# Performance work log

Hardware: AMD Instinct MI355X
Metric: run time of the kernel (lower is better)

The kernel has to match this reference:

```python
import jax, jax.numpy as jnp
import numpy as np

T, H, W = 64, 1024, 1024
GRAD_PCT = 0.15
BZ_PCT = 0.3      # 30th percentile of |Bz|


def setup_inputs() -> dict:
    key = jax.random.key(0)
    k1, k2, k3 = jax.random.split(key, 3)
    frames = jax.random.normal(k1, (T, H, W), dtype=jnp.float32)
    observed_mask = jnp.ones((T,), dtype=bool)
    conv_w = jax.random.normal(k2, (4, 1, 3), dtype=jnp.float32) * 0.3  # depthwise OIH
    conv_b = jax.random.normal(k3, (4,), dtype=jnp.float32) * 0.1
    return {"frames": frames, "observed_mask": observed_mask,
            "conv_w": conv_w, "conv_b": conv_b}


def _pil_stats(frames):
    # frames: [T,H,W] -> stats [T,4] (length, intensity, x_centroid, y_centroid)
    T_, H_, W_ = frames.shape
    N = H_ * W_
    gx = jnp.pad(frames[:, :, 1:] - frames[:, :, :-1], ((0, 0), (0, 0), (0, 1)))
    gy = jnp.pad(frames[:, 1:, :] - frames[:, :-1, :], ((0, 0), (0, 1), (0, 0)))
    gm = jnp.sqrt(gx * gx + gy * gy)                    # [T,H,W]
    gm_flat = gm.reshape(T_, N)
    thr = jnp.sort(gm_flat, axis=-1)[:, int((1.0 - GRAD_PCT) * (N - 1))]
    bz_abs = jnp.abs(frames).reshape(T_, N)
    bz_thr = jnp.sort(bz_abs, axis=-1)[:, int(BZ_PCT * (N - 1))]
    mask = ((gm_flat > thr[:, None]) & (bz_abs < bz_thr[:, None])).astype(frames.dtype)
    pil_sum = jnp.clip(mask.sum(-1), 1e-6)
    length = pil_sum / N
    intensity = (gm_flat * mask).sum(-1) / pil_sum
    w3 = (mask * gm_flat).reshape(T_, H_, W_)           # centroid weights
    wsum = jnp.clip(w3.sum((1, 2)), 1e-6)
    xs = jnp.arange(W_, dtype=frames.dtype)
    ys = jnp.arange(H_, dtype=frames.dtype)
    x_cent = jnp.einsum('thw,w->t', w3, xs) / wsum / W_
    y_cent = jnp.einsum('thw,h->t', w3, ys) / wsum / H_
    return jnp.stack([length, intensity, x_cent, y_cent], axis=-1)


def reference(frames, observed_mask, conv_w, conv_b):
    # observed_mask is all-True -> all T frames observed (static n_obs = T)
    n = frames.shape[0]
    stats = _pil_stats(frames)                          # [T,4]
    x = stats.T[None]                                   # [1,4,T]
    y = jax.lax.conv_general_dilated(
        x, conv_w, window_strides=(1,), padding=((1, 1),),
        feature_group_count=4, dimension_numbers=('NCH', 'OIH', 'NCH'))
    s = (y + conv_b[None, :, None])[0].T                # [T,4] smoothed
    length, intensity, x_cent, y_cent = s[:, 0], s[:, 1], s[:, 2], s[:, 3]
    length_mean = length.mean()
    intensity_mean = intensity.mean()
    t_norm = jnp.linspace(0.0, 1.0, n)
    length_trend = ((length - length_mean) * (t_norm - 0.5)).sum() * 6 / n
    intensity_trend = ((intensity - intensity_mean) * (t_norm - 0.5)).sum() * 6 / n
    dx = x_cent[1:] - x_cent[:-1]
    dy = y_cent[1:] - y_cent[:-1]
    speeds = jnp.sqrt(dx * dx + dy * dy)
    motion_speed = speeds.mean()
    motion_direction = jnp.arctan2(dy.sum(), dx.sum()) / np.pi
    growth_rate = (length[-1] - length[0]) / max(1, n - 1)
    instability = jnp.std(speeds, ddof=1)               # unbiased, per-step speeds
    return jnp.stack([length_mean, length_trend, intensity_mean, intensity_trend,
                      motion_speed, motion_direction, growth_rate, instability])
```

## Files before the change

kernel.cpp:

```cpp
#include <hip/hip_runtime.h>
#include <math.h>
#include <stddef.h>

constexpr int T_ = 64;
constexpr int H_ = 1024;
constexpr int W_ = 1024;
constexpr int N_ = H_ * W_;
constexpr unsigned RANK_G = 891288;
constexpr unsigned RANK_B = 314572;

constexpr int ROWS_PER_BLOCK = 32;
constexpr int BLOCKS_PER_FRAME = H_ / ROWS_PER_BLOCK;

constexpr int SROWS = 16;
constexpr int NS = SROWS * W_;
constexpr int SHB = 8192;
constexpr int MARGIN = 192;
constexpr int RS_G = (int)(RANK_G / 64);
constexpr int RS_B = (int)(RANK_B / 64);

constexpr unsigned CAPG = 1536;
constexpr unsigned CAPB = 1536;
constexpr unsigned CAPX = 448;

constexpr unsigned CACHE_N = 26624;
constexpr int SEL_THREADS = 512;

constexpr int RES_SPLIT = 8;

struct WS {
  unsigned lo[2][T_], hi[2][T_];
  unsigned cntG[T_][32], cntB[T_][32], cntX[T_][32];
  unsigned cbG[T_][32], cbB[T_][32];
  float    thr[2][T_];
  double   part[T_][32][4];
  double   acc2[T_][RES_SPLIT][4];
  unsigned Gg[T_][32][CAPG];
  unsigned Ga[T_][32][CAPG];
  unsigned Bb[T_][32][CAPB];
  unsigned Xg[T_][32][CAPX];
  unsigned Xb[T_][32][CAPX];
  unsigned Xa[T_][32][CAPX];
};

__device__ __forceinline__ float gm_at(float cur, float right, float down,
                                       int col, int row) {
  float gx = (col < W_ - 1) ? (right - cur) : 0.0f;
  float gy = (row < H_ - 1) ? (down - cur) : 0.0f;
  return sqrtf(gx * gx + gy * gy);
}

__global__ __launch_bounds__(256) void sample_kernel(const float* __restrict__ frames,
                                                     WS* ws) {
  const int t = blockIdx.x;
  __shared__ unsigned hist[2][SHB];
  __shared__ unsigned sub[4][1024];
  __shared__ unsigned partial[256], chunk_before[256];
  __shared__ unsigned selB[4], selCB[4];
  const int tx = threadIdx.x, c = tx * 4;
  for (int i = tx; i < 2 * SHB; i += 256) (&hist[0][0])[i] = 0;
  for (int i = tx; i < 4 * 1024; i += 256) (&sub[0][0])[i] = 0;
  __syncthreads();
  const float* f = frames + (size_t)t * N_;

  for (int r = 0; r < SROWS; ++r) {
    const int h = r * 64 + 32;
    const float* row = f + (size_t)h * W_;
    float4 a = *(const float4*)(row + c);
    float an = (c + 4 < W_) ? row[c + 4] : 0.0f;
    float4 b = *(const float4*)(row + W_ + c);
    float xs[5] = {a.x, a.y, a.z, a.w, an};
    float ys[4] = {b.x, b.y, b.z, b.w};
#pragma unroll
    for (int j = 0; j < 4; ++j) {
      float gm = gm_at(xs[j], xs[j + 1], ys[j], c + j, h);
      float bz = fabsf(xs[j]);
      atomicAdd(&hist[0][__float_as_uint(gm) >> 18], 1u);
      atomicAdd(&hist[1][__float_as_uint(bz) >> 18], 1u);
    }
  }
  __syncthreads();

  for (int q = 0; q < 2; ++q) {
    unsigned s = 0;
    for (int j = 0; j < SHB / 256; ++j) s += hist[q][tx * (SHB / 256) + j];
    partial[tx] = s;
    __syncthreads();
    if (tx == 0) {
      unsigned cum = 0;
      for (int i = 0; i < 256; ++i) { chunk_before[i] = cum; cum += partial[i]; }
    }
    __syncthreads();
    for (int e = 0; e < 2; ++e) {
      int k = (q == 0 ? RS_G : RS_B) + (e == 0 ? -MARGIN : MARGIN);
      unsigned cb = chunk_before[tx];
      if ((unsigned)k >= cb && (unsigned)k < cb + partial[tx]) {
        unsigned rem = (unsigned)k - cb, cum = 0;
        for (int j = 0; j < SHB / 256; ++j) {
          unsigned hv = hist[q][tx * (SHB / 256) + j];
          if (rem < cum + hv) {
            selB[q * 2 + e]  = tx * (SHB / 256) + j;
            selCB[q * 2 + e] = cb + cum;
            break;
          }
          cum += hv;
        }
      }
    }
    __syncthreads();
  }

  for (int r = 0; r < SROWS; ++r) {
    const int h = r * 64 + 32;
    const float* row = f + (size_t)h * W_;
    float4 a = *(const float4*)(row + c);
    float an = (c + 4 < W_) ? row[c + 4] : 0.0f;
    float4 b = *(const float4*)(row + W_ + c);
    float xs[5] = {a.x, a.y, a.z, a.w, an};
    float ys[4] = {b.x, b.y, b.z, b.w};
#pragma unroll
    for (int j = 0; j < 4; ++j) {
      float gm = gm_at(xs[j], xs[j + 1], ys[j], c + j, h);
      float bz = fabsf(xs[j]);
      unsigned ug = __float_as_uint(gm), ub = __float_as_uint(bz);
#pragma unroll
      for (int e = 0; e < 2; ++e) {
        if ((ug >> 18) == selB[e])     atomicAdd(&sub[e][(ug >> 8) & 1023u], 1u);
        if ((ub >> 18) == selB[2 + e]) atomicAdd(&sub[2 + e][(ub >> 8) & 1023u], 1u);
      }
    }
  }
  __syncthreads();

  for (int qe = 0; qe < 4; ++qe) {
    unsigned s = 0;
    for (int j = 0; j < 4; ++j) s += sub[qe][tx * 4 + j];
    partial[tx] = s;
    __syncthreads();
    if (tx == 0) {
      unsigned cum = 0;
      for (int i = 0; i < 256; ++i) { chunk_before[i] = cum; cum += partial[i]; }
    }
    __syncthreads();
    int q = qe >> 1, e = qe & 1;
    int k0 = (q == 0 ? RS_G : RS_B) + (e == 0 ? -MARGIN : MARGIN);
    unsigned k = (unsigned)k0 - selCB[qe];
    unsigned cb = chunk_before[tx];
    if (k >= cb && k < cb + partial[tx]) {
      unsigned rem = k - cb, cum = 0;
      for (int j = 0; j < 4; ++j) {
        unsigned hv = sub[qe][tx * 4 + j];
        if (rem < cum + hv) {
          unsigned sb = tx * 4 + j;
          unsigned bound = (selB[qe] << 18) | (sb << 8);
          if (e == 0) ws->lo[q][t] = bound;
          else        ws->hi[q][t] = bound + 256u;
          break;
        }
        cum += hv;
      }
    }
    __syncthreads();
  }
}

__global__ __launch_bounds__(256) void main_kernel(const float* __restrict__ frames,
                                                   WS* ws) {
  const int t = blockIdx.y, blk = blockIdx.x, r0 = blk * ROWS_PER_BLOCK;
  const unsigned lg = ws->lo[0][t], hg = ws->hi[0][t];
  const unsigned lb = ws->lo[1][t], hb = ws->hi[1][t];
  __shared__ unsigned cnt[3];
  const int tx = threadIdx.x, c = tx * 4, lane = tx & 63, wave = tx >> 6;
  if (tx < 3) cnt[tx] = 0;
  __syncthreads();
  unsigned* __restrict__ Gg = ws->Gg[t][blk];
  unsigned* __restrict__ Ga = ws->Ga[t][blk];
  unsigned* __restrict__ Bb = ws->Bb[t][blk];
  unsigned* __restrict__ Xg = ws->Xg[t][blk];
  unsigned* __restrict__ Xb = ws->Xb[t][blk];
  unsigned* __restrict__ Xa = ws->Xa[t][blk];
  const float* f = frames + (size_t)t * N_;

  unsigned cbg = 0, cbb = 0;
  float s0 = 0.f, s1 = 0.f, s2 = 0.f, s3 = 0.f;

  const float* row0 = f + (size_t)r0 * W_;
  float4 a = *(const float4*)(row0 + c);
  float an = (c + 4 < W_) ? row0[c + 4] : 0.0f;

  for (int r = 0; r < ROWS_PER_BLOCK; ++r) {
    const int h = r0 + r;
    float4 b; float bn;
    if (h + 1 < H_) {
      const float* rowN = f + (size_t)(h + 1) * W_;
      b  = *(const float4*)(rowN + c);
      bn = (c + 4 < W_) ? rowN[c + 4] : 0.0f;
    } else {
      b = a; bn = an;
    }
    float xs[5] = {a.x, a.y, a.z, a.w, an};
    float ys[4] = {b.x, b.y, b.z, b.w};
#pragma unroll
    for (int j = 0; j < 4; ++j) {
      float gm = gm_at(xs[j], xs[j + 1], ys[j], c + j, h);
      float bz = fabsf(xs[j]);
      unsigned ug = __float_as_uint(gm);
      unsigned ub = __float_as_uint(bz);
      bool bz_lo = (ub < lb);
      if (ug < lg) {
        cbg++;
      } else if (ug < hg) {
        unsigned o = atomicAdd(&cnt[0], 1u);
        if (o < CAPG) {
          Gg[o] = ug;
          Ga[o] = (unsigned)(c + j) | ((unsigned)h << 10) | (bz_lo ? (1u << 20) : 0u);
        }
      }
      if (bz_lo) {
        cbb++;
        if (ug >= hg) {
          s0 += 1.0f; s1 += gm;
          s2 += gm * (float)(c + j); s3 += gm * (float)h;
        }
      } else if (ub < hb) {
        unsigned o = atomicAdd(&cnt[1], 1u);
        if (o < CAPB) Bb[o] = ub;
        if (ug >= lg) {
          unsigned o2 = atomicAdd(&cnt[2], 1u);
          if (o2 < CAPX) {
            Xg[o2] = ug; Xb[o2] = ub;
            Xa[o2] = (unsigned)(c + j) | ((unsigned)h << 10);
          }
        }
      }
    }
    a = b; an = bn;
  }

  for (int off = 32; off; off >>= 1) {
    cbg += __shfl_down(cbg, off);
    cbb += __shfl_down(cbb, off);
    s0  += __shfl_down(s0, off);
    s1  += __shfl_down(s1, off);
    s2  += __shfl_down(s2, off);
    s3  += __shfl_down(s3, off);
  }
  __shared__ unsigned wcb[2][4];
  __shared__ float wss[4][4];
  if (lane == 0) {
    wcb[0][wave] = cbg; wcb[1][wave] = cbb;
    wss[0][wave] = s0; wss[1][wave] = s1; wss[2][wave] = s2; wss[3][wave] = s3;
  }
  __syncthreads();
  if (tx == 0) {
    ws->cbG[t][blk] = wcb[0][0] + wcb[0][1] + wcb[0][2] + wcb[0][3];
    ws->cbB[t][blk] = wcb[1][0] + wcb[1][1] + wcb[1][2] + wcb[1][3];
    ws->part[t][blk][0] = (double)wss[0][0] + wss[0][1] + wss[0][2] + wss[0][3];
    ws->part[t][blk][1] = (double)wss[1][0] + wss[1][1] + wss[1][2] + wss[1][3];
    ws->part[t][blk][2] = (double)wss[2][0] + wss[2][1] + wss[2][2] + wss[2][3];
    ws->part[t][blk][3] = (double)wss[3][0] + wss[3][1] + wss[3][2] + wss[3][3];
    ws->cntG[t][blk] = min(cnt[0], CAPG);
    ws->cntB[t][blk] = min(cnt[1], CAPB);
    ws->cntX[t][blk] = min(cnt[2], CAPX);
  }
}

__global__ __launch_bounds__(SEL_THREADS) void select_kernel(WS* ws) {
  const int t = blockIdx.x, q = blockIdx.y, tx = threadIdx.x;
  __shared__ unsigned cache[CACHE_N];
  __shared__ unsigned hist[2048];
  __shared__ unsigned partial[SEL_THREADS], chunk_before[SEL_THREADS];
  __shared__ unsigned nseg[32], segbase[33];
  __shared__ unsigned sel[2];
  __shared__ unsigned shrank;
  const unsigned lo = ws->lo[q][t];
  const unsigned hi = ws->hi[q][t];
  if (tx < 32) nseg[tx] = (q == 0) ? ws->cntG[t][tx] : ws->cntB[t][tx];
  __syncthreads();
  if (tx == 0) {
    unsigned cb = 0, base = 0;
    for (int i = 0; i < 32; ++i) {
      segbase[i] = base; base += nseg[i];
      cb += (q == 0) ? ws->cbG[t][i] : ws->cbB[t][i];
    }
    segbase[32] = base;
    long long rk = (long long)((q == 0) ? RANK_G : RANK_B) - (long long)cb;
    if (rk < 0) rk = 0;
    if (base > 0 && rk >= (long long)base) rk = (long long)base - 1;
    shrank = (unsigned)rk;
  }
  __syncthreads();
  const unsigned total = segbase[32];
  if (total == 0) {
    if (tx == 0) ws->thr[q][t] = __uint_as_float(lo);
    return;
  }
  const unsigned range = hi - lo;
  const int w = 32 - __clz(range | 1u);
  int sp = (w > 11) ? (w - 11) : 0;
  unsigned rank = shrank, base_val = 0;
  unsigned flt_span = 0xFFFFFFFFu;
  bool first = true;

  while (true) {
    for (int i = tx; i < 2048; i += SEL_THREADS) hist[i] = 0;
    __syncthreads();

    if (first) {
      for (int blk = 0; blk < 32; ++blk) {
        const unsigned n = nseg[blk], sb = segbase[blk];
        const unsigned* __restrict__ ptr = (q == 0) ? ws->Gg[t][blk] : ws->Bb[t][blk];
        for (unsigned i = tx; i < n; i += SEL_THREADS) {
          unsigned d = ptr[i] - lo;
          unsigned slot = sb + i;
          if (slot < CACHE_N) cache[slot] = d;
          atomicAdd(&hist[d >> sp], 1u);
        }
      }
    } else {
      const unsigned lim = (total < CACHE_N) ? total : CACHE_N;
      for (unsigned i = tx; i < lim; i += SEL_THREADS) {
        unsigned rel = cache[i] - base_val;
        if (rel < flt_span) atomicAdd(&hist[rel >> sp], 1u);
      }
      if (total > CACHE_N) {
        for (int blk = 0; blk < 32; ++blk) {
          const unsigned sb = segbase[blk], n = nseg[blk];
          if (sb + n <= CACHE_N) continue;
          const unsigned start = (sb < CACHE_N) ? (CACHE_N - sb) : 0;
          const unsigned* __restrict__ ptr = (q == 0) ? ws->Gg[t][blk] : ws->Bb[t][blk];
          for (unsigned i = start + tx; i < n; i += SEL_THREADS) {
            unsigned rel = (ptr[i] - lo) - base_val;
            if (rel < flt_span) atomicAdd(&hist[rel >> sp], 1u);
          }
        }
      }
    }
    __syncthreads();

    unsigned s = 0;
#pragma unroll
    for (int j = 0; j < 2048 / SEL_THREADS; ++j) s += hist[tx * (2048 / SEL_THREADS) + j];
    partial[tx] = s;
    __syncthreads();
    if (tx == 0) {
      unsigned cum = 0;
      for (int i = 0; i < SEL_THREADS; ++i) { chunk_before[i] = cum; cum += partial[i]; }
    }
    __syncthreads();
    unsigned cb2 = chunk_before[tx];
    if (rank >= cb2 && rank < cb2 + partial[tx]) {
      unsigned rem = rank - cb2, cum = 0;
#pragma unroll
      for (int j = 0; j < 2048 / SEL_THREADS; ++j) {
        unsigned hv = hist[tx * (2048 / SEL_THREADS) + j];
        if (rem < cum + hv) { sel[0] = tx * (2048 / SEL_THREADS) + j; sel[1] = rem - cum; break; }
        cum += hv;
      }
    }
    __syncthreads();
    rank = sel[1];
    base_val += sel[0] << sp;
    if (sp == 0) {
      if (tx == 0) ws->thr[q][t] = __uint_as_float(lo + base_val);
      break;
    }
    flt_span = 1u << sp;
    sp = (sp > 11) ? (sp - 11) : 0;
    first = false;
    __syncthreads();
  }
}

__global__ __launch_bounds__(256) void resolve_kernel(WS* ws) {
  const int t = blockIdx.x, p = blockIdx.y, tx = threadIdx.x;
  const unsigned tg = __float_as_uint(ws->thr[0][t]);
  const unsigned tb = __float_as_uint(ws->thr[1][t]);
  float c = 0.f, sg = 0.f, sx = 0.f, sy = 0.f;
  for (int blk = p * 4; blk < p * 4 + 4; ++blk) {
    const unsigned nG = ws->cntG[t][blk];
    const unsigned* __restrict__ Gg = ws->Gg[t][blk];
    const unsigned* __restrict__ Ga = ws->Ga[t][blk];
    for (unsigned i = tx; i < nG; i += 256) {
      unsigned g = Gg[i], a = Ga[i];
      if (g > tg && (a & (1u << 20))) {
        float v = __uint_as_float(g);
        c += 1.f; sg += v;
        sx += v * (float)(a & 1023u);
        sy += v * (float)((a >> 10) & 1023u);
      }
    }
    const unsigned nX = ws->cntX[t][blk];
    const unsigned* __restrict__ Xg = ws->Xg[t][blk];
    const unsigned* __restrict__ Xb = ws->Xb[t][blk];
    const unsigned* __restrict__ Xa = ws->Xa[t][blk];
    for (unsigned i = tx; i < nX; i += 256) {
      unsigned g = Xg[i], bb = Xb[i], a = Xa[i];
      if (g > tg && bb < tb) {
        float v = __uint_as_float(g);
        c += 1.f; sg += v;
        sx += v * (float)(a & 1023u);
        sy += v * (float)((a >> 10) & 1023u);
      }
    }
  }
  double dc = c, dg = sg, dx = sx, dy = sy;
  if (tx < 4) {
    const double* pp = ws->part[t][p * 4 + tx];
    dc += pp[0]; dg += pp[1]; dx += pp[2]; dy += pp[3];
  }
  for (int off = 32; off; off >>= 1) {
    dc += __shfl_down(dc, off);
    dg += __shfl_down(dg, off);
    dx += __shfl_down(dx, off);
    dy += __shfl_down(dy, off);
  }
  __shared__ double pd[4][4];
  const int wave = tx >> 6, lane = tx & 63;
  if (lane == 0) { pd[0][wave] = dc; pd[1][wave] = dg; pd[2][wave] = dx; pd[3][wave] = dy; }
  __syncthreads();
  if (tx == 0) {
    ws->acc2[t][p][0] = pd[0][0] + pd[0][1] + pd[0][2] + pd[0][3];
    ws->acc2[t][p][1] = pd[1][0] + pd[1][1] + pd[1][2] + pd[1][3];
    ws->acc2[t][p][2] = pd[2][0] + pd[2][1] + pd[2][2] + pd[2][3];
    ws->acc2[t][p][3] = pd[3][0] + pd[3][1] + pd[3][2] + pd[3][3];
  }
}

__global__ __launch_bounds__(64) void finalize_kernel(WS* ws,
                                                      const float* __restrict__ conv_w,
                                                      const float* __restrict__ conv_b,
                                                      float* __restrict__ out) {
  __shared__ float st[T_][4];
  __shared__ float s[T_][4];
  const int tx = threadIdx.x;
  if (tx < T_) {
    double cnt = 0.0, sgm = 0.0, swx = 0.0, swy = 0.0;
#pragma unroll
    for (int b = 0; b < RES_SPLIT; ++b) {
      cnt += ws->acc2[tx][b][0];
      sgm += ws->acc2[tx][b][1];
      swx += ws->acc2[tx][b][2];
      swy += ws->acc2[tx][b][3];
    }
    float pil  = fmaxf((float)cnt, 1e-6f);
    float wsum = fmaxf((float)sgm, 1e-6f);
    st[tx][0] = pil / (float)N_;
    st[tx][1] = (float)sgm / pil;
    st[tx][2] = (float)swx / wsum / (float)W_;
    st[tx][3] = (float)swy / wsum / (float)H_;
  }
  __syncthreads();
  if (tx < T_) {
#pragma unroll
    for (int c2 = 0; c2 < 4; ++c2) {
      float acc = conv_b[c2];
#pragma unroll
      for (int k = 0; k < 3; ++k) {
        int ti = tx + k - 1;
        if (ti >= 0 && ti < T_) acc += conv_w[c2 * 3 + k] * st[ti][c2];
      }
      s[tx][c2] = acc;
    }
  }
  __syncthreads();
  if (tx == 0) {
    float lm = 0.f, im = 0.f;
    for (int i = 0; i < T_; ++i) { lm += s[i][0]; im += s[i][1]; }
    lm /= (float)T_; im /= (float)T_;
    float lt = 0.f, it = 0.f;
    for (int i = 0; i < T_; ++i) {
      float tn = (float)i / (float)(T_ - 1) - 0.5f;
      lt += (s[i][0] - lm) * tn;
      it += (s[i][1] - im) * tn;
    }
    lt *= 6.0f / (float)T_;
    it *= 6.0f / (float)T_;
    float speeds[T_ - 1];
    float spsum = 0.f, sdx = 0.f, sdy = 0.f;
    for (int i = 0; i < T_ - 1; ++i) {
      float dx = s[i + 1][2] - s[i][2];
      float dy = s[i + 1][3] - s[i][3];
      float sp = sqrtf(dx * dx + dy * dy);
      speeds[i] = sp; spsum += sp; sdx += dx; sdy += dy;
    }
    float ms  = spsum / (float)(T_ - 1);
    float dir = atan2f(sdy, sdx) / 3.14159265358979323846f;
    float gr  = (s[T_ - 1][0] - s[0][0]) / (float)(T_ - 1);
    float var = 0.f;
    for (int i = 0; i < T_ - 1; ++i) { float d = speeds[i] - ms; var += d * d; }
    float inst = sqrtf(var / (float)(T_ - 2));
    out[0] = lm; out[1] = lt; out[2] = im; out[3] = it;
    out[4] = ms; out[5] = dir; out[6] = gr; out[7] = inst;
  }
}

extern "C" void kernel_launch(void* const* d_in, const int* in_sizes, int n_in,
                              void* d_out, int out_size, void* d_ws, size_t ws_size,
                              hipStream_t stream) {
  const float* frames = (const float*)d_in[0];
  const float* conv_w = (const float*)d_in[2];
  const float* conv_b = (const float*)d_in[3];
  float* out = (float*)d_out;
  WS* ws = (WS*)d_ws;


  sample_kernel<<<T_, 256, 0, stream>>>(frames, ws);
  main_kernel<<<dim3(BLOCKS_PER_FRAME, T_), 256, 0, stream>>>(frames, ws);
  select_kernel<<<dim3(T_, 2), SEL_THREADS, 0, stream>>>(ws);
  resolve_kernel<<<dim3(T_, RES_SPLIT), 256, 0, stream>>>(ws);
  finalize_kernel<<<1, 64, 0, stream>>>(ws, conv_w, conv_b, out);
}
```

Measured before the change: 513.3 us.

## Replace serial prefix scans with wave-shuffle scans, shuffle neighbor loads, nontemporal loads

Replaces the single-thread serial exclusive scans over 256/512 partial sums in the sample and select kernels with a wave-level shuffle scan followed by a cross-wave combine. Neighbor column values are now taken with a lane shuffle instead of an extra scalar global load, and only the last lane still reads memory directly. The main kernel uses nontemporal vector loads, and several loops get unroll pragmas. Together these aim to cut serialized scan latency and redundant memory traffic, at the cost of shuffle overhead and a scan helper that relies on barriers being reached by every thread.

```diff
diff --git a/kernel.cpp b/kernel.cpp
--- a/kernel.cpp
+++ b/kernel.cpp
@@ -27,6 +27,8 @@
 constexpr int SEL_THREADS = 512;
 
 constexpr int RES_SPLIT = 8;
+
+typedef float f4_t __attribute__((ext_vector_type(4)));
 
 struct WS {
   unsigned lo[2][T_], hi[2][T_];
@@ -50,25 +52,47 @@
   return sqrtf(gx * gx + gy * gy);
 }
 
+template <int NT>
+__device__ __forceinline__ unsigned excl_scan_block(unsigned v, int tx,
+                                                    volatile unsigned* wsum) {
+  const int lane = tx & 63, wv = tx >> 6;
+  unsigned s = v;
+#pragma unroll
+  for (int o = 1; o < 64; o <<= 1) {
+    unsigned u = __shfl_up(s, o);
+    if (lane >= o) s += u;
+  }
+  if (lane == 63) wsum[wv] = s;
+  __syncthreads();
+  unsigned base = 0;
+#pragma unroll
+  for (int w = 0; w < NT / 64; ++w)
+    if (w < wv) base += wsum[w];
+  __syncthreads();
+  return base + s - v;
+}
+
 __global__ __launch_bounds__(256) void sample_kernel(const float* __restrict__ frames,
                                                      WS* ws) {
   const int t = blockIdx.x;
   __shared__ unsigned hist[2][SHB];
   __shared__ unsigned sub[4][1024];
-  __shared__ unsigned partial[256], chunk_before[256];
+  __shared__ unsigned wscan[4];
   __shared__ unsigned selB[4], selCB[4];
-  const int tx = threadIdx.x, c = tx * 4;
+  const int tx = threadIdx.x, c = tx * 4, lane = tx & 63;
   for (int i = tx; i < 2 * SHB; i += 256) (&hist[0][0])[i] = 0;
   for (int i = tx; i < 4 * 1024; i += 256) (&sub[0][0])[i] = 0;
   __syncthreads();
   const float* f = frames + (size_t)t * N_;
 
+#pragma unroll 4
   for (int r = 0; r < SROWS; ++r) {
     const int h = r * 64 + 32;
     const float* row = f + (size_t)h * W_;
-    float4 a = *(const float4*)(row + c);
-    float an = (c + 4 < W_) ? row[c + 4] : 0.0f;
-    float4 b = *(const float4*)(row + W_ + c);
+    f4_t a = *(const f4_t*)(row + c);
+    f4_t b = *(const f4_t*)(row + W_ + c);
+    float an = __shfl_down(a.x, 1);
+    if (lane == 63) an = (c + 4 < W_) ? row[c + 4] : 0.0f;
     float xs[5] = {a.x, a.y, a.z, a.w, an};
     float ys[4] = {b.x, b.y, b.z, b.w};
 #pragma unroll
@@ -83,18 +107,13 @@
 
   for (int q = 0; q < 2; ++q) {
     unsigned s = 0;
+#pragma unroll
     for (int j = 0; j < SHB / 256; ++j) s += hist[q][tx * (SHB / 256) + j];
-    partial[tx] = s;
-    __syncthreads();
-    if (tx == 0) {
-      unsigned cum = 0;
-      for (int i = 0; i < 256; ++i) { chunk_before[i] = cum; cum += partial[i]; }
-    }
-    __syncthreads();
+    unsigned cb = excl_scan_block<256>(s, tx, wscan);
+#pragma unroll
     for (int e = 0; e < 2; ++e) {
       int k = (q == 0 ? RS_G : RS_B) + (e == 0 ? -MARGIN : MARGIN);
-      unsigned cb = chunk_before[tx];
-      if ((unsigned)k >= cb && (unsigned)k < cb + partial[tx]) {
+      if ((unsigned)k >= cb && (unsigned)k < cb + s) {
         unsigned rem = (unsigned)k - cb, cum = 0;
         for (int j = 0; j < SHB / 256; ++j) {
           unsigned hv = hist[q][tx * (SHB / 256) + j];
@@ -110,12 +129,14 @@
     __syncthreads();
   }
 
+#pragma unroll 4
   for (int r = 0; r < SROWS; ++r) {
     const int h = r * 64 + 32;
     const float* row = f + (size_t)h * W_;
-    float4 a = *(const float4*)(row + c);
-    float an = (c + 4 < W_) ? row[c + 4] : 0.0f;
-    float4 b = *(const float4*)(row + W_ + c);
+    f4_t a = *(const f4_t*)(row + c);
+    f4_t b = *(const f4_t*)(row + W_ + c);
+    float an = __shfl_down(a.x, 1);
+    if (lane == 63) an = (c + 4 < W_) ? row[c + 4] : 0.0f;
     float xs[5] = {a.x, a.y, a.z, a.w, an};
     float ys[4] = {b.x, b.y, b.z, b.w};
 #pragma unroll
@@ -134,19 +155,13 @@
 
   for (int qe = 0; qe < 4; ++qe) {
     unsigned s = 0;
+#pragma unroll
     for (int j = 0; j < 4; ++j) s += sub[qe][tx * 4 + j];
-    partial[tx] = s;
-    __syncthreads();
-    if (tx == 0) {
-      unsigned cum = 0;
-      for (int i = 0; i < 256; ++i) { chunk_before[i] = cum; cum += partial[i]; }
-    }
-    __syncthreads();
+    unsigned cb = excl_scan_block<256>(s, tx, wscan);
     int q = qe >> 1, e = qe & 1;
     int k0 = (q == 0 ? RS_G : RS_B) + (e == 0 ? -MARGIN : MARGIN);
     unsigned k = (unsigned)k0 - selCB[qe];
-    unsigned cb = chunk_before[tx];
-    if (k >= cb && k < cb + partial[tx]) {
+    if (k >= cb && k < cb + s) {
       unsigned rem = k - cb, cum = 0;
       for (int j = 0; j < 4; ++j) {
         unsigned hv = sub[qe][tx * 4 + j];
@@ -185,16 +200,19 @@
   float s0 = 0.f, s1 = 0.f, s2 = 0.f, s3 = 0.f;
 
   const float* row0 = f + (size_t)r0 * W_;
-  float4 a = *(const float4*)(row0 + c);
-  float an = (c + 4 < W_) ? row0[c + 4] : 0.0f;
-
+  f4_t a = __builtin_nontemporal_load((const f4_t*)(row0 + c));
+  float an = __shfl_down(a.x, 1);
+  if (lane == 63) an = (c + 4 < W_) ? row0[c + 4] : 0.0f;
+
+#pragma unroll 2
   for (int r = 0; r < ROWS_PER_BLOCK; ++r) {
     const int h = r0 + r;
-    float4 b; float bn;
+    f4_t b; float bn;
     if (h + 1 < H_) {
       const float* rowN = f + (size_t)(h + 1) * W_;
-      b  = *(const float4*)(rowN + c);
-      bn = (c + 4 < W_) ? rowN[c + 4] : 0.0f;
+      b  = __builtin_nontemporal_load((const f4_t*)(rowN + c));
+      bn = __shfl_down(b.x, 1);
+      if (lane == 63) bn = (c + 4 < W_) ? rowN[c + 4] : 0.0f;
     } else {
       b = a; bn = an;
     }
@@ -269,7 +287,7 @@
   const int t = blockIdx.x, q = blockIdx.y, tx = threadIdx.x;
   __shared__ unsigned cache[CACHE_N];
   __shared__ unsigned hist[2048];
-  __shared__ unsigned partial[SEL_THREADS], chunk_before[SEL_THREADS];
+  __shared__ unsigned wscan[SEL_THREADS / 64];
   __shared__ unsigned nseg[32], segbase[33];
   __shared__ unsigned sel[2];
   __shared__ unsigned shrank;
@@ -341,15 +359,8 @@
     unsigned s = 0;
 #pragma unroll
     for (int j = 0; j < 2048 / SEL_THREADS; ++j) s += hist[tx * (2048 / SEL_THREADS) + j];
-    partial[tx] = s;
-    __syncthreads();
-    if (tx == 0) {
-      unsigned cum = 0;
-      for (int i = 0; i < SEL_THREADS; ++i) { chunk_before[i] = cum; cum += partial[i]; }
-    }
-    __syncthreads();
-    unsigned cb2 = chunk_before[tx];
-    if (rank >= cb2 && rank < cb2 + partial[tx]) {
+    unsigned cb2 = excl_scan_block<SEL_THREADS>(s, tx, wscan);
+    if (rank >= cb2 && rank < cb2 + s) {
       unsigned rem = rank - cb2, cum = 0;
 #pragma unroll
       for (int j = 0; j < 2048 / SEL_THREADS; ++j) {
```

Result: faster. 502.7 us (-2.1%).
